# Performance work log

Measured on AMD Instinct MI355X. Metric: run time of the kernel, lower is better.

The kernel has to match this reference:

```python
import jax, jax.numpy as jnp
import numpy as np
import math

EPS = 1e-5

def _ln(x, w, b):
    m = jnp.mean(x, axis=-1, keepdims=True)
    v = jnp.mean((x - m) ** 2, axis=-1, keepdims=True)
    return (x - m) * jax.lax.rsqrt(v + EPS) * w + b

def setup_inputs() -> dict:
    key = jax.random.key(0)
    L, E, V, T, B = 8, 1024, 32000, 1024, 4
    ks = jax.random.split(key, 9)
    f = lambda k, s: jax.random.normal(k, s, dtype=jnp.float32) * 0.02
    return dict(
        idx=jax.random.randint(ks[0], (B, T), 0, V),
        wte=f(ks[1], (V, E)),
        wpe=f(ks[2], (T, E)),
        ln1_w=jnp.ones((L, E), jnp.float32), ln1_b=jnp.zeros((L, E), jnp.float32),
        attn_w=f(ks[3], (L, 3 * E, E)), attn_b=jnp.zeros((L, 3 * E), jnp.float32),
        proj_w=f(ks[4], (L, E, E)), proj_b=jnp.zeros((L, E), jnp.float32),
        ln2_w=jnp.ones((L, E), jnp.float32), ln2_b=jnp.zeros((L, E), jnp.float32),
        fc_w=f(ks[5], (L, 4 * E, E)), fc_b=jnp.zeros((L, 4 * E), jnp.float32),
        fc2_w=f(ks[6], (L, E, 4 * E)), fc2_b=jnp.zeros((L, E), jnp.float32),
        lnf_w=jnp.ones((E,), jnp.float32), lnf_b=jnp.zeros((E,), jnp.float32),
        lm_head_w=f(ks[7], (V, E)),
        n_head=16,
    )

def reference(idx, wte, wpe, ln1_w, ln1_b, attn_w, attn_b, proj_w, proj_b,
              ln2_w, ln2_b, fc_w, fc_b, fc2_w, fc2_b, lnf_w, lnf_b,
              lm_head_w, n_head):
    B, T = idx.shape
    E = wte.shape[1]
    H = int(n_head)
    hd = E // H
    scale = 1.0 / math.sqrt(hd)
    x = wte[idx] + wpe[:T]  # [B,T,E]
    causal = jnp.tril(jnp.ones((T, T), dtype=bool))
    neg_inf = jnp.float32(-jnp.inf)

    def body(x, p):
        l1w, l1b, Wa, ba, Wp, bp, l2w, l2b, Wf, bf, W2, b2 = p
        h = _ln(x, l1w, l1b)
        qkv = h @ Wa.T + ba  # [B,T,3E]
        q, k, v = jnp.split(qkv, 3, axis=-1)
        q = q.reshape(B, T, H, hd)
        k = k.reshape(B, T, H, hd)
        v = v.reshape(B, T, H, hd)
        att = jnp.einsum('bqhd,bkhd->bhqk', q, k) * scale
        att = jnp.where(causal, att, neg_inf)
        att = jax.nn.softmax(att, axis=-1)  # dropout is identity in eval
        y = jnp.einsum('bhqk,bkhd->bqhd', att, v).reshape(B, T, E)
        x = x + (y @ Wp.T + bp)
        h2 = _ln(x, l2w, l2b)
        mlp = jax.nn.gelu(h2 @ Wf.T + bf, approximate=False) @ W2.T + b2
        return x + mlp, None

    params = (ln1_w, ln1_b, attn_w, attn_b, proj_w, proj_b,
              ln2_w, ln2_b, fc_w, fc_b, fc2_w, fc2_b)
    x, _ = jax.lax.scan(body, x, params)
    x = _ln(x, lnf_w, lnf_b)
    logits = x @ lm_head_w.T  # [B,T,V]
    return logits
```

## Files before the change

### kernel.cpp

```cpp
#include <hip/hip_runtime.h>

typedef __bf16 bf16x8 __attribute__((ext_vector_type(8)));
typedef float  f32x4  __attribute__((ext_vector_type(4)));
typedef short  s16x8  __attribute__((ext_vector_type(8)));
typedef unsigned int u32;
#define AS1 __attribute__((address_space(1)))
#define AS3 __attribute__((address_space(3)))

#define E_ 1024
#define T_ 1024
#define B_ 4
#define L_ 8
#define V_ 32000
#define M_ (B_*T_)

static __device__ __forceinline__ ushort f2bf(float f) {
  return __builtin_bit_cast(ushort, (__bf16)f);
}

static __device__ __forceinline__ bf16x8 dsr(const ushort* p) {
  u32 a = (u32)(size_t)(const AS3 ushort*)p;
  bf16x8 d;
  asm volatile("ds_read_b128 %0, %1" : "=v"(d) : "v"(a));
  return d;
}

__global__ __launch_bounds__(256) void castall_k(
    const float* __restrict__ a0, const float* __restrict__ a1,
    const float* __restrict__ a2, const float* __restrict__ a3,
    const float* __restrict__ a4,
    ushort* __restrict__ o0, ushort* __restrict__ o1, ushort* __restrict__ o2,
    ushort* __restrict__ o3, ushort* __restrict__ o4) {
  int bid = blockIdx.x;
  const float* in; ushort* out; int base;
  if (bid < 12288)      { in = a0; out = o0; base = bid; }
  else if (bid < 16384) { in = a1; out = o1; base = bid - 12288; }
  else if (bid < 32768) { in = a2; out = o2; base = bid - 16384; }
  else if (bid < 49152) { in = a3; out = o3; base = bid - 32768; }
  else                  { in = a4; out = o4; base = bid - 49152; }
  size_t i = ((size_t)base * 256 + threadIdx.x) * 8;
  float4 a = *(const float4*)(in + i);
  float4 b = *(const float4*)(in + i + 4);
  float v[8] = {a.x, a.y, a.z, a.w, b.x, b.y, b.z, b.w};
  union { s16x8 v; ushort u[8]; } pk;
  #pragma unroll
  for (int j = 0; j < 8; ++j) pk.u[j] = f2bf(v[j]);
  *(s16x8*)(out + i) = pk.v;
}

static __device__ __forceinline__ void ln_core(float4 v, int t,
    const float* __restrict__ w, const float* __restrict__ b,
    ushort* __restrict__ out, size_t row) {
  float s  = v.x + v.y + v.z + v.w;
  float s2 = v.x*v.x + v.y*v.y + v.z*v.z + v.w*v.w;
  #pragma unroll
  for (int o = 32; o > 0; o >>= 1) { s += __shfl_down(s, o); s2 += __shfl_down(s2, o); }
  __shared__ float sh[8];
  int wv = t >> 6;
  if ((t & 63) == 0) { sh[wv] = s; sh[4 + wv] = s2; }
  __syncthreads();
  s  = sh[0] + sh[1] + sh[2] + sh[3];
  s2 = sh[4] + sh[5] + sh[6] + sh[7];
  float mean = s * (1.f / E_);
  float var  = s2 * (1.f / E_) - mean * mean;
  float inv  = rsqrtf(var + 1e-5f);
  float4 wv4 = ((const float4*)w)[t];
  float4 bv4 = ((const float4*)b)[t];
  ushort* op = out + row * E_ + t * 4;
  op[0] = f2bf((v.x - mean) * inv * wv4.x + bv4.x);
  op[1] = f2bf((v.y - mean) * inv * wv4.y + bv4.y);
  op[2] = f2bf((v.z - mean) * inv * wv4.z + bv4.z);
  op[3] = f2bf((v.w - mean) * inv * wv4.w + bv4.w);
}

__global__ __launch_bounds__(256) void embedln_k(const int* __restrict__ idx,
    const float* __restrict__ wte, const float* __restrict__ wpe,
    const float* __restrict__ w, const float* __restrict__ b,
    float* __restrict__ x, ushort* __restrict__ out) {
  int row = blockIdx.x;
  int tok = idx[row];
  int t = row & (T_ - 1);
  int c = threadIdx.x;
  float4 a = ((const float4*)(wte + (size_t)tok * E_))[c];
  float4 p = ((const float4*)(wpe + (size_t)t * E_))[c];
  float4 v; v.x = a.x + p.x; v.y = a.y + p.y; v.z = a.z + p.z; v.w = a.w + p.w;
  ((float4*)(x + (size_t)row * E_))[c] = v;
  ln_core(v, c, w, b, out, (size_t)row);
}

__global__ __launch_bounds__(256) void ln_k(const float* __restrict__ x,
    const float* __restrict__ w, const float* __restrict__ b,
    ushort* __restrict__ out) {
  int row = blockIdx.x;
  int t = threadIdx.x;
  float4 v = ((const float4*)(x + (size_t)row * E_))[t];
  ln_core(v, t, w, b, out, (size_t)row);
}

__global__ __launch_bounds__(256) void redln_k(const float* __restrict__ p,
    const float* __restrict__ bias, float* __restrict__ x,
    const float* __restrict__ w, const float* __restrict__ b,
    ushort* __restrict__ out) {
  int row = blockIdx.x;
  int t = threadIdx.x;
  float4 v = ((const float4*)(x + (size_t)row * E_))[t];
  float4 bb = ((const float4*)bias)[t];
  v.x += bb.x; v.y += bb.y; v.z += bb.z; v.w += bb.w;
  #pragma unroll
  for (int sk = 0; sk < 4; ++sk) {
    float4 q = ((const float4*)(p + ((size_t)sk * M_ + row) * E_))[t];
    v.x += q.x; v.y += q.y; v.z += q.z; v.w += q.w;
  }
  ((float4*)(x + (size_t)row * E_))[t] = v;
  ln_core(v, t, w, b, out, (size_t)row);
}

template<int BUF, int MH, int NH, int RA, int RB, int VM, typename F>
static __device__ __forceinline__ void ph8(
    const ushort* AL, const ushort* BL,
    bf16x8 (&av)[2][4][2], bf16x8 (&bv)[2][2][2],
    int arow, int brow, int ca0, int ca1, f32x4 (&acc)[8][4], F&& stage) {
  if (RA) {
    #pragma unroll
    for (int mfi = 0; mfi < 4; ++mfi) {
      av[MH][mfi][0] = dsr(&AL[(BUF*2+MH)*8192 + arow + mfi*1024 + ca0]);
      av[MH][mfi][1] = dsr(&AL[(BUF*2+MH)*8192 + arow + mfi*1024 + ca1]);
    }
  }
  if (RB) {
    #pragma unroll
    for (int nfi = 0; nfi < 2; ++nfi) {
      bv[NH][nfi][0] = dsr(&BL[(BUF*2+NH)*8192 + brow + nfi*1024 + ca0]);
      bv[NH][nfi][1] = dsr(&BL[(BUF*2+NH)*8192 + brow + nfi*1024 + ca1]);
    }
  }
  stage();
  __builtin_amdgcn_s_barrier();
  asm volatile("s_waitcnt lgkmcnt(0)");
  __builtin_amdgcn_sched_barrier(0);
  __builtin_amdgcn_s_setprio(1);
  #pragma unroll
  for (int ks = 0; ks < 2; ++ks)
    #pragma unroll
    for (int mfi = 0; mfi < 4; ++mfi)
      #pragma unroll
      for (int nfi = 0; nfi < 2; ++nfi)
        acc[MH*4+mfi][NH*2+nfi] = __builtin_amdgcn_mfma_f32_16x16x32_bf16(
            av[MH][mfi][ks], bv[NH][nfi][ks], acc[MH*4+mfi][NH*2+nfi], 0, 0, 0);
  __builtin_amdgcn_s_setprio(0);
  if (VM) asm volatile("s_waitcnt vmcnt(4)");
  __builtin_amdgcn_s_barrier();
  __builtin_amdgcn_sched_barrier(0);
}

#define GLDS(src, dst) __builtin_amdgcn_global_load_lds((const AS1 u32*)(src), (AS3 u32*)(dst), 16, 0, 0)
#define STAGE_A(b, s, t) do { \
  GLDS(ap##s##_0 + (size_t)(t)*64, &AL[((b)*2+(s))*8192 + w*512]); \
  GLDS(ap##s##_1 + (size_t)(t)*64, &AL[((b)*2+(s))*8192 + 4096 + w*512]); } while(0)
#define STAGE_B(b, s, t) do { \
  GLDS(bp##s##_0 + (size_t)(t)*64, &BL[((b)*2+(s))*8192 + w*512]); \
  GLDS(bp##s##_1 + (size_t)(t)*64, &BL[((b)*2+(s))*8192 + 4096 + w*512]); } while(0)

template<int EPI>
static __device__ __forceinline__
void gemm8_body(const ushort* __restrict__ A, const ushort* __restrict__ W,
                const float* __restrict__ bias,
                float* __restrict__ outf, ushort* __restrict__ outh,
                ushort* __restrict__ qb, ushort* __restrict__ kb, ushort* __restrict__ vb,
                int M, int N, int K, int Kst) {
  __shared__ __align__(16) ushort AL[32768];
  __shared__ __align__(16) ushort BL[32768];
  int id  = blockIdx.x;
  int sk = 0, bx, by;
  if (EPI == 4) {
    sk = id >> 6; int rem = id & 63; bx = rem & 3; by = rem >> 2;
  } else {
    int nwg = gridDim.x;
    int swz = (id & 7) * (nwg >> 3) + (id >> 3);
    bx = swz >> 4; by = swz & 15;
  }
  int bm = by * 256, bn = bx * 256;
  int tid = threadIdx.x;
  int w = tid >> 6, lane = tid & 63;
  int wm = w >> 2, wn = w & 3;
  int g = lane >> 4, lr = lane & 15;
  int sl8 = lane >> 3, sc = lane & 7;
  int cg8 = (sc ^ sl8) * 8;

  const ushort* Ab = A + (size_t)sk * K;
  const ushort* Wb = W + (size_t)sk * K;
  int r0 = w * 8 + sl8;
  const ushort* ap0_0 = Ab + (size_t)(bm +       0 + r0) * Kst + cg8;
  const ushort* ap0_1 = Ab + (size_t)(bm + 128 + 0 + r0) * Kst + cg8;
  const ushort* ap1_0 = Ab + (size_t)(bm +      64 + r0) * Kst + cg8;
  const ushort* ap1_1 = Ab + (size_t)(bm + 128 + 64 + r0) * Kst + cg8;
  int sr0 = r0, sr1 = 64 + r0;
  const ushort* bp0_0 = Wb + (size_t)(bn + (sr0 >> 5) * 64 +  0 + (sr0 & 31)) * Kst + cg8;
  const ushort* bp0_1 = Wb + (size_t)(bn + (sr1 >> 5) * 64 +  0 + (sr1 & 31)) * Kst + cg8;
  const ushort* bp1_0 = Wb + (size_t)(bn + (sr0 >> 5) * 64 + 32 + (sr0 & 31)) * Kst + cg8;
  const ushort* bp1_1 = Wb + (size_t)(bn + (sr1 >> 5) * 64 + 32 + (sr1 & 31)) * Kst + cg8;

  int NT = K >> 6;
  int NITER = NT >> 1;
  int arow = (wm * 64 + lr) * 64;
  int brow = (wn * 32 + lr) * 64;
  int ca0 = ((0 + g) ^ (lr & 7)) * 8;
  int ca1 = ((4 + g) ^ (lr & 7)) * 8;
  f32x4 acc[8][4] = {};
  bf16x8 av[2][4][2], bv[2][2][2];

  STAGE_A(0, 0, 0); STAGE_A(0, 1, 0); STAGE_B(0, 0, 0); STAGE_B(0, 1, 0);
  STAGE_A(1, 0, 1); STAGE_B(1, 0, 1);
  asm volatile("s_waitcnt vmcnt(0)" ::: "memory");
  __builtin_amdgcn_s_barrier();
  __builtin_amdgcn_sched_barrier(0);

  for (int i = 0; i < NITER; ++i) {
    int t1 = 2 * i + 1;
    int t2 = 2 * i + 2; if (t2 > NT - 1) t2 = NT - 1;
    int t3 = 2 * i + 3; if (t3 > NT - 1) t3 = NT - 1;
    ph8<0,0,0,1,1,0>(AL, BL, av, bv, arow, brow, ca0, ca1, acc, [&]{ STAGE_A(1, 1, t1); });
    ph8<0,0,1,0,1,0>(AL, BL, av, bv, arow, brow, ca0, ca1, acc, [&]{ STAGE_B(1, 1, t1); });
    ph8<0,1,1,1,0,0>(AL, BL, av, bv, arow, brow, ca0, ca1, acc, [&]{ STAGE_A(0, 0, t2); });
    ph8<0,1,0,0,0,1>(AL, BL, av, bv, arow, brow, ca0, ca1, acc, [&]{ STAGE_B(0, 0, t2); });
    ph8<1,0,0,1,1,0>(AL, BL, av, bv, arow, brow, ca0, ca1, acc, [&]{ STAGE_A(0, 1, t2); });
    ph8<1,0,1,0,1,0>(AL, BL, av, bv, arow, brow, ca0, ca1, acc, [&]{ STAGE_B(0, 1, t2); });
    ph8<1,1,1,1,0,0>(AL, BL, av, bv, arow, brow, ca0, ca1, acc, [&]{ STAGE_A(1, 0, t3); });
    ph8<1,1,0,0,0,1>(AL, BL, av, bv, arow, brow, ca0, ca1, acc, [&]{ STAGE_B(1, 0, t3); });
  }

  if (EPI == 3 && (bn >> 10) == 2) {
    #pragma unroll
    for (int mf = 0; mf < 8; ++mf) {
      int row = bm + wm * 128 + mf * 16 + g * 4;
      int b = row >> 10, t = row & 1023;
      #pragma unroll
      for (int nf = 0; nf < 4; ++nf) {
        int col = bn + wn * 64 + nf * 16 + lr;
        int cc = col & 1023;
        int h = cc >> 6, d = cc & 63;
        float bs = bias[col];
        union { ushort u[4]; uint2 v; } pk4;
        #pragma unroll
        for (int reg = 0; reg < 4; ++reg) pk4.u[reg] = f2bf(acc[mf][nf][reg] + bs);
        *(uint2*)&vb[((size_t)(b * 16 + h) * 64 + d) * T_ + t] = pk4.v;
      }
    }
    return;
  }

  ushort* dst = nullptr; float scl = 1.f;
  if (EPI == 3) {
    int sec = bn >> 10;
    dst = (sec == 0) ? qb : kb;
    scl = (sec == 0) ? 0.125f : 1.f;
  }
  #pragma unroll
  for (int mf = 0; mf < 8; ++mf) {
    #pragma unroll
    for (int reg = 0; reg < 4; ++reg) {
      int row = bm + wm * 128 + mf * 16 + g * 4 + reg;
      #pragma unroll
      for (int nf = 0; nf < 4; ++nf) {
        int col = bn + wn * 64 + nf * 16 + lr;
        float v = acc[mf][nf][reg];
        if (bias) v += bias[col];
        if (EPI == 0) {
          outf[(size_t)row * N + col] = v;
        } else if (EPI == 2) {
          float gl = 0.5f * v * (1.f + erff(v * 0.70710678118654752f));
          outh[(size_t)row * N + col] = f2bf(gl);
        } else if (EPI == 4) {
          outf[((size_t)sk * M + row) * N + col] = v;
        } else {
          int b = row >> 10, t = row & 1023;
          int cc = col & 1023;
          int h = cc >> 6, d = cc & 63;
          dst[((size_t)(b * 16 + h) * T_ + t) * 64 + d] = f2bf(v * scl);
        }
      }
    }
  }
}

__global__ __launch_bounds__(512, 2)
void gemm8_qkv(const ushort* A, const ushort* W, const float* bias,
               ushort* qb, ushort* kb, ushort* vtb) {
  gemm8_body<3>(A, W, bias, nullptr, nullptr, qb, kb, vtb, M_, 3 * E_, E_, E_);
}
__global__ __launch_bounds__(512, 2)
void gemm8_fc(const ushort* A, const ushort* W, const float* bias, ushort* outh) {
  gemm8_body<2>(A, W, bias, nullptr, outh, nullptr, nullptr, nullptr, M_, 4 * E_, E_, E_);
}
__global__ __launch_bounds__(512, 2)
void gemm8_lm(const ushort* A, const ushort* W, float* outf) {
  gemm8_body<0>(A, W, nullptr, outf, nullptr, nullptr, nullptr, nullptr, M_, V_, E_, E_);
}
__global__ __launch_bounds__(512, 2)
void gemm8_sk(const ushort* A, const ushort* W, float* pbuf) {
  gemm8_body<4>(A, W, nullptr, pbuf, nullptr, nullptr, nullptr, nullptr, M_, E_, E_, 4 * E_);
}

__global__ __launch_bounds__(256, 4)
void gbt2_proj(const ushort* __restrict__ A, const ushort* __restrict__ W,
               const float* __restrict__ bias, const float* __restrict__ res,
               float* __restrict__ outf) {
  __shared__ __align__(16) ushort As[128 * 64];
  __shared__ __align__(16) ushort Ws[128 * 64];
  const int N = E_, K = E_;
  int id  = blockIdx.x;
  int nwg = gridDim.x;
  int swz = (id & 7) * (nwg >> 3) + (id >> 3);
  int bx = swz >> 5, by = swz & 31;
  int bm = by * 128, bn = bx * 128;
  int tid  = threadIdx.x;
  int wave = tid >> 6, lane = tid & 63;
  int wr = wave >> 1, wc = wave & 1;
  int g  = lane >> 4, lr = lane & 15;
  int sl8 = lane >> 3, sc = lane & 7;
  int cg8 = (sc ^ sl8) * 8;
  int r0 = wave * 8 + sl8;

  const ushort* ap = A + (size_t)(bm + r0) * K + cg8;
  const ushort* wp = W + (size_t)(bn + r0) * K + cg8;
  f32x4 acc[4][4] = {};

  for (int k0 = 0; k0 < K; k0 += 64) {
    #pragma unroll
    for (int j = 0; j < 4; ++j) {
      GLDS(ap + (size_t)(j * 32) * K + k0, &As[(wave * 8 + j * 32) * 64]);
      GLDS(wp + (size_t)(j * 32) * K + k0, &Ws[(wave * 8 + j * 32) * 64]);
    }
    __syncthreads();
    #pragma unroll
    for (int ks = 0; ks < 2; ++ks) {
      int ca = ((ks * 4 + g) ^ (lr & 7)) * 8;
      bf16x8 af[4], bfr[4];
      #pragma unroll
      for (int f = 0; f < 4; ++f) {
        af[f]  = __builtin_bit_cast(bf16x8, *(const s16x8*)&As[(wr * 64 + f * 16 + lr) * 64 + ca]);
        bfr[f] = __builtin_bit_cast(bf16x8, *(const s16x8*)&Ws[(wc * 64 + f * 16 + lr) * 64 + ca]);
      }
      #pragma unroll
      for (int mf = 0; mf < 4; ++mf)
        #pragma unroll
        for (int nf = 0; nf < 4; ++nf)
          acc[mf][nf] = __builtin_amdgcn_mfma_f32_16x16x32_bf16(af[mf], bfr[nf], acc[mf][nf], 0, 0, 0);
    }
    __syncthreads();
  }

  #pragma unroll
  for (int mf = 0; mf < 4; ++mf)
    #pragma unroll
    for (int reg = 0; reg < 4; ++reg) {
      int row = bm + wr * 64 + mf * 16 + g * 4 + reg;
      #pragma unroll
      for (int nf = 0; nf < 4; ++nf) {
        int col = bn + wc * 64 + nf * 16 + lr;
        float v = acc[mf][nf][reg] + bias[col];
        outf[(size_t)row * N + col] = v + res[(size_t)row * N + col];
      }
    }
}

static __device__ __forceinline__ void sm_step(
    f32x4 (&s)[4], float& m, float& l, f32x4 (&acc)[4], bf16x8 (&ap)[2],
    int qrow, int kbase0, bool diag, int g) {
  if (diag) {
    #pragma unroll
    for (int nf = 0; nf < 4; ++nf)
      #pragma unroll
      for (int reg = 0; reg < 4; ++reg)
        if (kbase0 + nf * 16 + g * 4 + reg > qrow) s[nf][reg] = -INFINITY;
  }
  float pmax = s[0][0];
  #pragma unroll
  for (int nf = 0; nf < 4; ++nf)
    #pragma unroll
    for (int reg = 0; reg < 4; ++reg) pmax = fmaxf(pmax, s[nf][reg]);
  pmax = fmaxf(pmax, __shfl_xor(pmax, 16));
  pmax = fmaxf(pmax, __shfl_xor(pmax, 32));
  if (__any(pmax > m + 8.f)) {
    float mn = fmaxf(m, pmax);
    float corr = __expf(m - mn);
    m = mn; l *= corr;
    #pragma unroll
    for (int reg = 0; reg < 4; ++reg) {
      float cc = __shfl(corr, g * 4 + reg);
      #pragma unroll
      for (int nfd = 0; nfd < 4; ++nfd) acc[nfd][reg] *= cc;
    }
  }
  float ps = 0.f;
  union { bf16x8 v[2]; ushort u[16]; } pk;
  #pragma unroll
  for (int nf = 0; nf < 4; ++nf)
    #pragma unroll
    for (int reg = 0; reg < 4; ++reg) {
      float pv = __expf(s[nf][reg] - m);
      ps += pv;
      pk.u[nf * 4 + reg] = f2bf(pv);
    }
  ps += __shfl_xor(ps, 16);
  ps += __shfl_xor(ps, 32);
  l += ps;
  ap[0] = pk.v[0];
  ap[1] = pk.v[1];
}

__global__ __launch_bounds__(256) void attn4_k(const ushort* __restrict__ Qg,
    const ushort* __restrict__ Kg, const ushort* __restrict__ Vg,
    ushort* __restrict__ y) {
  __shared__ __align__(16) ushort KL[2][4096];
  __shared__ __align__(16) ushort VL[2][4096];
  int bh = blockIdx.x;
  int qt = blockIdx.y;
  int tid = threadIdx.x, w = tid >> 6, lane = tid & 63;
  int g = lane >> 4, lr = lane & 15;
  int sl8 = lane >> 3, sc = lane & 7;
  int cg8 = (sc ^ sl8) * 8;
  int qbase = qt * 128 + w * 32;

  const ushort* kbase = Kg + (size_t)bh * T_ * 64;
  const ushort* vbase = Vg + (size_t)bh * 64 * T_;

  bf16x8 aq[2][2];
  #pragma unroll
  for (int st = 0; st < 2; ++st) {
    const ushort* qp = Qg + ((size_t)bh * T_ + qbase + st * 16 + lr) * 64;
    aq[st][0] = __builtin_bit_cast(bf16x8, *(const s16x8*)(qp + g * 8));
    aq[st][1] = __builtin_bit_cast(bf16x8, *(const s16x8*)(qp + 32 + g * 8));
  }

  f32x4 accO[2][4] = {};
  float m0 = -INFINITY, m1 = -INFINITY, l0 = 0.f, l1 = 0.f;

  int nkt_blk = 2 * qt + 2;
  int nw = ((qbase + 31) >> 6) + 1;
  int r8 = w * 8 + sl8;

  #define STG_KV(buf, kt) do { \
    _Pragma("unroll") \
    for (int j_ = 0; j_ < 2; ++j_) { \
      GLDS(kbase + (size_t)((kt) * 64 + j_ * 32 + r8) * 64 + cg8, &KL[buf][(j_ * 32 + w * 8) * 64]); \
      GLDS(vbase + (size_t)(j_ * 32 + r8) * T_ + (kt) * 64 + cg8, &VL[buf][(j_ * 32 + w * 8) * 64]); \
    } \
  } while (0)

  STG_KV(0, 0);
  __syncthreads();

  for (int kt = 0; kt < nkt_blk; ++kt) {
    int cbuf = kt & 1;
    if (kt + 1 < nkt_blk) STG_KV(cbuf ^ 1, kt + 1);

    if (kt < nw) {
      bool diag = (kt == nw - 1);
      f32x4 s0[4] = {}, s1[4] = {};
      #pragma unroll
      for (int ks = 0; ks < 2; ++ks)
        #pragma unroll
        for (int nf = 0; nf < 4; ++nf) {
          int row = nf * 16 + lr;
          bf16x8 ak = __builtin_bit_cast(bf16x8,
              *(const s16x8*)&KL[cbuf][row * 64 + (((ks * 4 + g) ^ (lr & 7)) * 8)]);
          s0[nf] = __builtin_amdgcn_mfma_f32_16x16x32_bf16(ak, aq[0][ks], s0[nf], 0, 0, 0);
          s1[nf] = __builtin_amdgcn_mfma_f32_16x16x32_bf16(ak, aq[1][ks], s1[nf], 0, 0, 0);
        }

      bf16x8 ap0[2], ap1[2];
      sm_step(s0, m0, l0, accO[0], ap0, qbase + 0 * 16 + lr, kt * 64, diag, g);
      sm_step(s1, m1, l1, accO[1], ap1, qbase + 1 * 16 + lr, kt * 64, diag, g);

      #pragma unroll
      for (int ks = 0; ks < 2; ++ks)
        #pragma unroll
        for (int nfd = 0; nfd < 4; ++nfd) {
          int row = nfd * 16 + lr;
          int c1 = ks * 4 + (g >> 1), sub = (g & 1) * 4;
          uint2 lo = *(const uint2*)&VL[cbuf][row * 64 + ((c1 ^ (lr & 7)) * 8 + sub)];
          uint2 hi = *(const uint2*)&VL[cbuf][row * 64 + (((c1 + 2) ^ (lr & 7)) * 8 + sub)];
          union { uint4 u; bf16x8 v; } bb;
          bb.u = make_uint4(lo.x, lo.y, hi.x, hi.y);
          accO[0][nfd] = __builtin_amdgcn_mfma_f32_16x16x32_bf16(ap0[ks], bb.v, accO[0][nfd], 0, 0, 0);
          accO[1][nfd] = __builtin_amdgcn_mfma_f32_16x16x32_bf16(ap1[ks], bb.v, accO[1][nfd], 0, 0, 0);
        }
    }
    __syncthreads();
  }

  int b = bh >> 4, h = bh & 15;
  float li0 = 1.f / l0, li1 = 1.f / l1;
  #pragma unroll
  for (int st = 0; st < 2; ++st) {
    float lsrc = (st == 0) ? li0 : li1;
    #pragma unroll
    for (int reg = 0; reg < 4; ++reg) {
      float inv = __shfl(lsrc, g * 4 + reg);
      size_t row = (size_t)b * T_ + qbase + st * 16 + g * 4 + reg;
      #pragma unroll
      for (int nfd = 0; nfd < 4; ++nfd)
        y[row * E_ + h * 64 + nfd * 16 + lr] = f2bf(accO[st][nfd][reg] * inv);
    }
  }
  #undef STG_KV
}

extern "C" void kernel_launch(void* const* d_in, const int* in_sizes, int n_in,
                              void* d_out, int out_size, void* d_ws, size_t ws_size,
                              hipStream_t stream) {
  const int*   idx   = (const int*)  d_in[0];
  const float* wte   = (const float*)d_in[1];
  const float* wpe   = (const float*)d_in[2];
  const float* ln1w  = (const float*)d_in[3];
  const float* ln1b  = (const float*)d_in[4];
  const float* attnw = (const float*)d_in[5];
  const float* attnb = (const float*)d_in[6];
  const float* projw = (const float*)d_in[7];
  const float* projb = (const float*)d_in[8];
  const float* ln2w  = (const float*)d_in[9];
  const float* ln2b  = (const float*)d_in[10];
  const float* fcw   = (const float*)d_in[11];
  const float* fcb   = (const float*)d_in[12];
  const float* fc2w  = (const float*)d_in[13];
  const float* fc2b  = (const float*)d_in[14];
  const float* lnfw  = (const float*)d_in[15];
  const float* lnfb  = (const float*)d_in[16];
  const float* lmw   = (const float*)d_in[17];
  float* out = (float*)d_out;

  char* p = (char*)d_ws;
  auto take = [&](size_t bytes) { char* r = p; p += (bytes + 255) & ~(size_t)255; return r; };
  ushort* wb_attn = (ushort*)take((size_t)L_ * 3 * E_ * E_ * 2);
  ushort* wb_proj = (ushort*)take((size_t)L_ * E_ * E_ * 2);
  ushort* wb_fc   = (ushort*)take((size_t)L_ * 4 * E_ * E_ * 2);
  ushort* wb_fc2  = (ushort*)take((size_t)L_ * E_ * 4 * E_ * 2);
  ushort* wb_lm   = (ushort*)take((size_t)V_ * E_ * 2);
  float*  x       = (float*) take((size_t)M_ * E_ * 4);
  ushort* hbuf    = (ushort*)take((size_t)M_ * E_ * 2);
  ushort* qb      = (ushort*)take((size_t)B_ * 16 * T_ * 64 * 2);
  ushort* kbuf    = (ushort*)take((size_t)B_ * 16 * T_ * 64 * 2);
  ushort* vtb     = (ushort*)take((size_t)B_ * 16 * T_ * 64 * 2);
  ushort* ybuf    = (ushort*)take((size_t)M_ * E_ * 2);
  ushort* mlp     = (ushort*)take((size_t)M_ * 4 * E_ * 2);
  float*  pbuf    = (float*) take((size_t)4 * M_ * E_ * 4);

  castall_k<<<65152, 256, 0, stream>>>(attnw, projw, fcw, fc2w, lmw,
                                       wb_attn, wb_proj, wb_fc, wb_fc2, wb_lm);
  embedln_k<<<M_, 256, 0, stream>>>(idx, wte, wpe, ln1w, ln1b, x, hbuf);

  for (int l = 0; l < L_; ++l) {
    gemm8_qkv<<<(3 * E_ / 256) * (M_ / 256), 512, 0, stream>>>(
        hbuf, wb_attn + (size_t)l * 3 * E_ * E_, attnb + l * 3 * E_, qb, kbuf, vtb);
    attn4_k<<<dim3(B_ * 16, T_ / 128), 256, 0, stream>>>(qb, kbuf, vtb, ybuf);
    gbt2_proj<<<(E_ / 128) * (M_ / 128), 256, 0, stream>>>(
        ybuf, wb_proj + (size_t)l * E_ * E_, projb + l * E_, x, x);
    ln_k<<<M_, 256, 0, stream>>>(x, ln2w + l * E_, ln2b + l * E_, hbuf);
    gemm8_fc<<<(4 * E_ / 256) * (M_ / 256), 512, 0, stream>>>(
        hbuf, wb_fc + (size_t)l * 4 * E_ * E_, fcb + l * 4 * E_, mlp);
    gemm8_sk<<<256, 512, 0, stream>>>(mlp, wb_fc2 + (size_t)l * E_ * 4 * E_, pbuf);
    if (l < L_ - 1)
      redln_k<<<M_, 256, 0, stream>>>(pbuf, fc2b + l * E_, x,
                                      ln1w + (l + 1) * E_, ln1b + (l + 1) * E_, hbuf);
    else
      redln_k<<<M_, 256, 0, stream>>>(pbuf, fc2b + l * E_, x, lnfw, lnfb, hbuf);
  }
  gemm8_lm<<<(V_ / 256) * (M_ / 256), 512, 0, stream>>>(hbuf, wb_lm, out);
}
```

Before: 2.350 ms.

## Move layer GEMMs to simple 128x128 kernel and store split-K partials as bf16

The QKV, FC and FC2 split-K GEMMs move off the deeply pipelined 256x256, 512-thread kernel onto the simpler 128x128, 256-thread kernel already used for proj. That kernel is generalised with epilogue variants for residual add, GELU, QKV scatter and split-K. Split-K partials are now written as bf16 instead of fp32, halving partial-buffer traffic, and the reduce kernel widens them back to fp32. The simple kernel gives more workgroups and occupancy but loses the software pipelining, and bf16 partials lose some accuracy. Only the LM head keeps the pipelined kernel.

```diff
diff --git a/kernel.cpp b/kernel.cpp
--- a/kernel.cpp
+++ b/kernel.cpp
@@ -16,6 +16,10 @@
 
 static __device__ __forceinline__ ushort f2bf(float f) {
   return __builtin_bit_cast(ushort, (__bf16)f);
+}
+static __device__ __forceinline__ float bf2f(ushort u) {
+  u32 t = (u32)u << 16;
+  return __builtin_bit_cast(float, t);
 }
 
 static __device__ __forceinline__ bf16x8 dsr(const ushort* p) {
@@ -97,7 +101,7 @@
   ln_core(v, t, w, b, out, (size_t)row);
 }
 
-__global__ __launch_bounds__(256) void redln_k(const float* __restrict__ p,
+__global__ __launch_bounds__(256) void redln_k(const ushort* __restrict__ p,
     const float* __restrict__ bias, float* __restrict__ x,
     const float* __restrict__ w, const float* __restrict__ b,
     ushort* __restrict__ out) {
@@ -108,8 +112,8 @@
   v.x += bb.x; v.y += bb.y; v.z += bb.z; v.w += bb.w;
   #pragma unroll
   for (int sk = 0; sk < 4; ++sk) {
-    float4 q = ((const float4*)(p + ((size_t)sk * M_ + row) * E_))[t];
-    v.x += q.x; v.y += q.y; v.z += q.z; v.w += q.w;
+    const ushort* q = p + ((size_t)sk * M_ + row) * E_ + t * 4;
+    v.x += bf2f(q[0]); v.y += bf2f(q[1]); v.z += bf2f(q[2]); v.w += bf2f(q[3]);
   }
   ((float4*)(x + (size_t)row * E_))[t] = v;
   ln_core(v, t, w, b, out, (size_t)row);
@@ -161,24 +165,16 @@
   GLDS(bp##s##_0 + (size_t)(t)*64, &BL[((b)*2+(s))*8192 + w*512]); \
   GLDS(bp##s##_1 + (size_t)(t)*64, &BL[((b)*2+(s))*8192 + 4096 + w*512]); } while(0)
 
-template<int EPI>
-static __device__ __forceinline__
-void gemm8_body(const ushort* __restrict__ A, const ushort* __restrict__ W,
-                const float* __restrict__ bias,
-                float* __restrict__ outf, ushort* __restrict__ outh,
-                ushort* __restrict__ qb, ushort* __restrict__ kb, ushort* __restrict__ vb,
-                int M, int N, int K, int Kst) {
+__global__ __launch_bounds__(512, 2)
+void gemm8_lm(const ushort* __restrict__ A, const ushort* __restrict__ W,
+              float* __restrict__ outf) {
+  const int N = V_, K = E_, Kst = E_;
   __shared__ __align__(16) ushort AL[32768];
   __shared__ __align__(16) ushort BL[32768];
   int id  = blockIdx.x;
-  int sk = 0, bx, by;
-  if (EPI == 4) {
-    sk = id >> 6; int rem = id & 63; bx = rem & 3; by = rem >> 2;
-  } else {
-    int nwg = gridDim.x;
-    int swz = (id & 7) * (nwg >> 3) + (id >> 3);
-    bx = swz >> 4; by = swz & 15;
-  }
+  int nwg = gridDim.x;
+  int swz = (id & 7) * (nwg >> 3) + (id >> 3);
+  int bx = swz >> 4, by = swz & 15;
   int bm = by * 256, bn = bx * 256;
   int tid = threadIdx.x;
   int w = tid >> 6, lane = tid & 63;
@@ -187,18 +183,16 @@
   int sl8 = lane >> 3, sc = lane & 7;
   int cg8 = (sc ^ sl8) * 8;
 
-  const ushort* Ab = A + (size_t)sk * K;
-  const ushort* Wb = W + (size_t)sk * K;
   int r0 = w * 8 + sl8;
-  const ushort* ap0_0 = Ab + (size_t)(bm +       0 + r0) * Kst + cg8;
-  const ushort* ap0_1 = Ab + (size_t)(bm + 128 + 0 + r0) * Kst + cg8;
-  const ushort* ap1_0 = Ab + (size_t)(bm +      64 + r0) * Kst + cg8;
-  const ushort* ap1_1 = Ab + (size_t)(bm + 128 + 64 + r0) * Kst + cg8;
+  const ushort* ap0_0 = A + (size_t)(bm +       0 + r0) * Kst + cg8;
+  const ushort* ap0_1 = A + (size_t)(bm + 128 + 0 + r0) * Kst + cg8;
+  const ushort* ap1_0 = A + (size_t)(bm +      64 + r0) * Kst + cg8;
+  const ushort* ap1_1 = A + (size_t)(bm + 128 + 64 + r0) * Kst + cg8;
   int sr0 = r0, sr1 = 64 + r0;
-  const ushort* bp0_0 = Wb + (size_t)(bn + (sr0 >> 5) * 64 +  0 + (sr0 & 31)) * Kst + cg8;
-  const ushort* bp0_1 = Wb + (size_t)(bn + (sr1 >> 5) * 64 +  0 + (sr1 & 31)) * Kst + cg8;
-  const ushort* bp1_0 = Wb + (size_t)(bn + (sr0 >> 5) * 64 + 32 + (sr0 & 31)) * Kst + cg8;
-  const ushort* bp1_1 = Wb + (size_t)(bn + (sr1 >> 5) * 64 + 32 + (sr1 & 31)) * Kst + cg8;
+  const ushort* bp0_0 = W + (size_t)(bn + (sr0 >> 5) * 64 +  0 + (sr0 & 31)) * Kst + cg8;
+  const ushort* bp0_1 = W + (size_t)(bn + (sr1 >> 5) * 64 +  0 + (sr1 & 31)) * Kst + cg8;
+  const ushort* bp1_0 = W + (size_t)(bn + (sr0 >> 5) * 64 + 32 + (sr0 & 31)) * Kst + cg8;
+  const ushort* bp1_1 = W + (size_t)(bn + (sr1 >> 5) * 64 + 32 + (sr1 & 31)) * Kst + cg8;
 
   int NT = K >> 6;
   int NITER = NT >> 1;
@@ -229,14 +223,80 @@
     ph8<1,1,0,0,0,1>(AL, BL, av, bv, arow, brow, ca0, ca1, acc, [&]{ STAGE_B(1, 0, t3); });
   }
 
-  if (EPI == 3 && (bn >> 10) == 2) {
-    #pragma unroll
-    for (int mf = 0; mf < 8; ++mf) {
-      int row = bm + wm * 128 + mf * 16 + g * 4;
-      int b = row >> 10, t = row & 1023;
+  #pragma unroll
+  for (int mf = 0; mf < 8; ++mf)
+    #pragma unroll
+    for (int reg = 0; reg < 4; ++reg) {
+      int row = bm + wm * 128 + mf * 16 + g * 4 + reg;
       #pragma unroll
       for (int nf = 0; nf < 4; ++nf) {
         int col = bn + wn * 64 + nf * 16 + lr;
+        outf[(size_t)row * N + col] = acc[mf][nf][reg];
+      }
+    }
+}
+
+template<int EPI>
+static __device__ __forceinline__
+void gbt2_body(const ushort* __restrict__ A, const ushort* __restrict__ W,
+               const float* __restrict__ bias, const float* __restrict__ res,
+               float* __restrict__ outf, ushort* __restrict__ outh,
+               ushort* __restrict__ qb, ushort* __restrict__ kb, ushort* __restrict__ vb,
+               int N, int K, int Kst, int gx) {
+  __shared__ __align__(16) ushort As[128 * 64];
+  __shared__ __align__(16) ushort Ws[128 * 64];
+  int id  = blockIdx.x;
+  int nwg = gridDim.x;
+  int swz = (id & 7) * (nwg >> 3) + (id >> 3);
+  int sk = 0;
+  if (EPI == 4) { sk = swz >> 8; swz &= 255; }
+  int bx = swz / 32, by = swz & 31;
+  int bm = by * 128, bn = bx * 128;
+  int tid  = threadIdx.x;
+  int wave = tid >> 6, lane = tid & 63;
+  int wr = wave >> 1, wc = wave & 1;
+  int g  = lane >> 4, lr = lane & 15;
+  int sl8 = lane >> 3, sc = lane & 7;
+  int cg8 = (sc ^ sl8) * 8;
+  int r0 = wave * 8 + sl8;
+
+  const ushort* ap = A + (size_t)sk * 1024 + (size_t)(bm + r0) * Kst + cg8;
+  const ushort* wp = W + (size_t)sk * 1024 + (size_t)(bn + r0) * Kst + cg8;
+  f32x4 acc[4][4] = {};
+
+  for (int k0 = 0; k0 < K; k0 += 64) {
+    #pragma unroll
+    for (int j = 0; j < 4; ++j) {
+      GLDS(ap + (size_t)(j * 32) * Kst + k0, &As[(wave * 8 + j * 32) * 64]);
+      GLDS(wp + (size_t)(j * 32) * Kst + k0, &Ws[(wave * 8 + j * 32) * 64]);
+    }
+    __syncthreads();
+    #pragma unroll
+    for (int ks = 0; ks < 2; ++ks) {
+      int ca = ((ks * 4 + g) ^ (lr & 7)) * 8;
+      bf16x8 af[4], bfr[4];
+      #pragma unroll
+      for (int f = 0; f < 4; ++f) {
+        af[f]  = __builtin_bit_cast(bf16x8, *(const s16x8*)&As[(wr * 64 + f * 16 + lr) * 64 + ca]);
+        bfr[f] = __builtin_bit_cast(bf16x8, *(const s16x8*)&Ws[(wc * 64 + f * 16 + lr) * 64 + ca]);
+      }
+      #pragma unroll
+      for (int mf = 0; mf < 4; ++mf)
+        #pragma unroll
+        for (int nf = 0; nf < 4; ++nf)
+          acc[mf][nf] = __builtin_amdgcn_mfma_f32_16x16x32_bf16(af[mf], bfr[nf], acc[mf][nf], 0, 0, 0);
+    }
+    __syncthreads();
+  }
+
+  if (EPI == 3 && (bn >> 10) == 2) {
+    #pragma unroll
+    for (int mf = 0; mf < 4; ++mf) {
+      int row = bm + wr * 64 + mf * 16 + g * 4;
+      int b = row >> 10, t = row & 1023;
+      #pragma unroll
+      for (int nf = 0; nf < 4; ++nf) {
+        int col = bn + wc * 64 + nf * 16 + lr;
         int cc = col & 1023;
         int h = cc >> 6, d = cc & 63;
         float bs = bias[col];
@@ -256,22 +316,22 @@
     scl = (sec == 0) ? 0.125f : 1.f;
   }
   #pragma unroll
-  for (int mf = 0; mf < 8; ++mf) {
+  for (int mf = 0; mf < 4; ++mf)
     #pragma unroll
     for (int reg = 0; reg < 4; ++reg) {
-      int row = bm + wm * 128 + mf * 16 + g * 4 + reg;
+      int row = bm + wr * 64 + mf * 16 + g * 4 + reg;
       #pragma unroll
       for (int nf = 0; nf < 4; ++nf) {
-        int col = bn + wn * 64 + nf * 16 + lr;
+        int col = bn + wc * 64 + nf * 16 + lr;
         float v = acc[mf][nf][reg];
-        if (bias) v += bias[col];
-        if (EPI == 0) {
-          outf[(size_t)row * N + col] = v;
+        if (EPI != 4) v += bias[col];
+        if (EPI == 1) {
+          outf[(size_t)row * N + col] = v + res[(size_t)row * N + col];
         } else if (EPI == 2) {
           float gl = 0.5f * v * (1.f + erff(v * 0.70710678118654752f));
           outh[(size_t)row * N + col] = f2bf(gl);
         } else if (EPI == 4) {
-          outf[((size_t)sk * M + row) * N + col] = v;
+          outh[((size_t)sk * M_ + row) * N + col] = f2bf(v);
         } else {
           int b = row >> 10, t = row & 1023;
           int cc = col & 1023;
@@ -280,88 +340,25 @@
         }
       }
     }
-  }
-}
-
-__global__ __launch_bounds__(512, 2)
-void gemm8_qkv(const ushort* A, const ushort* W, const float* bias,
-               ushort* qb, ushort* kb, ushort* vtb) {
-  gemm8_body<3>(A, W, bias, nullptr, nullptr, qb, kb, vtb, M_, 3 * E_, E_, E_);
-}
-__global__ __launch_bounds__(512, 2)
-void gemm8_fc(const ushort* A, const ushort* W, const float* bias, ushort* outh) {
-  gemm8_body<2>(A, W, bias, nullptr, outh, nullptr, nullptr, nullptr, M_, 4 * E_, E_, E_);
-}
-__global__ __launch_bounds__(512, 2)
-void gemm8_lm(const ushort* A, const ushort* W, float* outf) {
-  gemm8_body<0>(A, W, nullptr, outf, nullptr, nullptr, nullptr, nullptr, M_, V_, E_, E_);
-}
-__global__ __launch_bounds__(512, 2)
-void gemm8_sk(const ushort* A, const ushort* W, float* pbuf) {
-  gemm8_body<4>(A, W, nullptr, pbuf, nullptr, nullptr, nullptr, nullptr, M_, E_, E_, 4 * E_);
 }
 
 __global__ __launch_bounds__(256, 4)
-void gbt2_proj(const ushort* __restrict__ A, const ushort* __restrict__ W,
-               const float* __restrict__ bias, const float* __restrict__ res,
-               float* __restrict__ outf) {
-  __shared__ __align__(16) ushort As[128 * 64];
-  __shared__ __align__(16) ushort Ws[128 * 64];
-  const int N = E_, K = E_;
-  int id  = blockIdx.x;
-  int nwg = gridDim.x;
-  int swz = (id & 7) * (nwg >> 3) + (id >> 3);
-  int bx = swz >> 5, by = swz & 31;
-  int bm = by * 128, bn = bx * 128;
-  int tid  = threadIdx.x;
-  int wave = tid >> 6, lane = tid & 63;
-  int wr = wave >> 1, wc = wave & 1;
-  int g  = lane >> 4, lr = lane & 15;
-  int sl8 = lane >> 3, sc = lane & 7;
-  int cg8 = (sc ^ sl8) * 8;
-  int r0 = wave * 8 + sl8;
-
-  const ushort* ap = A + (size_t)(bm + r0) * K + cg8;
-  const ushort* wp = W + (size_t)(bn + r0) * K + cg8;
-  f32x4 acc[4][4] = {};
-
-  for (int k0 = 0; k0 < K; k0 += 64) {
-    #pragma unroll
-    for (int j = 0; j < 4; ++j) {
-      GLDS(ap + (size_t)(j * 32) * K + k0, &As[(wave * 8 + j * 32) * 64]);
-      GLDS(wp + (size_t)(j * 32) * K + k0, &Ws[(wave * 8 + j * 32) * 64]);
-    }
-    __syncthreads();
-    #pragma unroll
-    for (int ks = 0; ks < 2; ++ks) {
-      int ca = ((ks * 4 + g) ^ (lr & 7)) * 8;
-      bf16x8 af[4], bfr[4];
-      #pragma unroll
-      for (int f = 0; f < 4; ++f) {
-        af[f]  = __builtin_bit_cast(bf16x8, *(const s16x8*)&As[(wr * 64 + f * 16 + lr) * 64 + ca]);
-        bfr[f] = __builtin_bit_cast(bf16x8, *(const s16x8*)&Ws[(wc * 64 + f * 16 + lr) * 64 + ca]);
-      }
-      #pragma unroll
-      for (int mf = 0; mf < 4; ++mf)
-        #pragma unroll
-        for (int nf = 0; nf < 4; ++nf)
-          acc[mf][nf] = __builtin_amdgcn_mfma_f32_16x16x32_bf16(af[mf], bfr[nf], acc[mf][nf], 0, 0, 0);
-    }
-    __syncthreads();
-  }
-
-  #pragma unroll
-  for (int mf = 0; mf < 4; ++mf)
-    #pragma unroll
-    for (int reg = 0; reg < 4; ++reg) {
-      int row = bm + wr * 64 + mf * 16 + g * 4 + reg;
-      #pragma unroll
-      for (int nf = 0; nf < 4; ++nf) {
-        int col = bn + wc * 64 + nf * 16 + lr;
-        float v = acc[mf][nf][reg] + bias[col];
-        outf[(size_t)row * N + col] = v + res[(size_t)row * N + col];
-      }
-    }
+void gbt2_qkv(const ushort* A, const ushort* W, const float* bias,
+              ushort* qb, ushort* kb, ushort* vtb) {
+  gbt2_body<3>(A, W, bias, nullptr, nullptr, nullptr, qb, kb, vtb, 3 * E_, E_, E_, 24);
+}
+__global__ __launch_bounds__(256, 4)
+void gbt2_fc(const ushort* A, const ushort* W, const float* bias, ushort* outh) {
+  gbt2_body<2>(A, W, bias, nullptr, nullptr, outh, nullptr, nullptr, nullptr, 4 * E_, E_, E_, 32);
+}
+__global__ __launch_bounds__(256, 4)
+void gbt2_sk(const ushort* A, const ushort* W, ushort* pbh) {
+  gbt2_body<4>(A, W, nullptr, nullptr, nullptr, pbh, nullptr, nullptr, nullptr, E_, E_, 4 * E_, 8);
+}
+__global__ __launch_bounds__(256, 4)
+void gbt2_proj(const ushort* A, const ushort* W, const float* bias,
+               const float* res, float* outf) {
+  gbt2_body<1>(A, W, bias, res, outf, nullptr, nullptr, nullptr, nullptr, E_, E_, E_, 8);
 }
 
 static __device__ __forceinline__ void sm_step(
@@ -544,27 +541,27 @@
   ushort* vtb     = (ushort*)take((size_t)B_ * 16 * T_ * 64 * 2);
   ushort* ybuf    = (ushort*)take((size_t)M_ * E_ * 2);
   ushort* mlp     = (ushort*)take((size_t)M_ * 4 * E_ * 2);
-  float*  pbuf    = (float*) take((size_t)4 * M_ * E_ * 4);
+  ushort* pbh     = (ushort*)take((size_t)4 * M_ * E_ * 2);
 
   castall_k<<<65152, 256, 0, stream>>>(attnw, projw, fcw, fc2w, lmw,
                                        wb_attn, wb_proj, wb_fc, wb_fc2, wb_lm);
   embedln_k<<<M_, 256, 0, stream>>>(idx, wte, wpe, ln1w, ln1b, x, hbuf);
 
   for (int l = 0; l < L_; ++l) {
-    gemm8_qkv<<<(3 * E_ / 256) * (M_ / 256), 512, 0, stream>>>(
+    gbt2_qkv<<<24 * 32, 256, 0, stream>>>(
         hbuf, wb_attn + (size_t)l * 3 * E_ * E_, attnb + l * 3 * E_, qb, kbuf, vtb);
     attn4_k<<<dim3(B_ * 16, T_ / 128), 256, 0, stream>>>(qb, kbuf, vtb, ybuf);
-    gbt2_proj<<<(E_ / 128) * (M_ / 128), 256, 0, stream>>>(
+    gbt2_proj<<<8 * 32, 256, 0, stream>>>(
         ybuf, wb_proj + (size_t)l * E_ * E_, projb + l * E_, x, x);
     ln_k<<<M_, 256, 0, stream>>>(x, ln2w + l * E_, ln2b + l * E_, hbuf);
-    gemm8_fc<<<(4 * E_ / 256) * (M_ / 256), 512, 0, stream>>>(
+    gbt2_fc<<<32 * 32, 256, 0, stream>>>(
         hbuf, wb_fc + (size_t)l * 4 * E_ * E_, fcb + l * 4 * E_, mlp);
-    gemm8_sk<<<256, 512, 0, stream>>>(mlp, wb_fc2 + (size_t)l * E_ * 4 * E_, pbuf);
+    gbt2_sk<<<4 * 8 * 32, 256, 0, stream>>>(mlp, wb_fc2 + (size_t)l * E_ * 4 * E_, pbh);
     if (l < L_ - 1)
-      redln_k<<<M_, 256, 0, stream>>>(pbuf, fc2b + l * E_, x,
+      redln_k<<<M_, 256, 0, stream>>>(pbh, fc2b + l * E_, x,
                                       ln1w + (l + 1) * E_, ln1b + (l + 1) * E_, hbuf);
     else
-      redln_k<<<M_, 256, 0, stream>>>(pbuf, fc2b + l * E_, x, lnfw, lnfb, hbuf);
+      redln_k<<<M_, 256, 0, stream>>>(pbh, fc2b + l * E_, x, lnfw, lnfb, hbuf);
   }
   gemm8_lm<<<(V_ / 256) * (M_ / 256), 512, 0, stream>>>(hbuf, wb_lm, out);
 }
```

Measured after the change: 2.190 ms (median of 2 runs). -6.8%, faster.
